# Kernel tuning notes

Hardware: AMD Instinct MI355X
Metric: run time of the kernel (lower is better)

The kernel has to match this reference:

```python
import jax, jax.numpy as jnp
import numpy as np

N_NODES = 100000
N_EDGES = 800000
IN_F, H_F, OUT_F = 512, 256, 64
N_EXPERTS = 4  # k = 1


def _normalize_edges(edge_index, n):
    """gcn_norm: add self loops, symmetric D^-1/2 A D^-1/2 edge weights."""
    loop = jnp.arange(n, dtype=edge_index.dtype)
    row = jnp.concatenate([edge_index[0], loop])
    col = jnp.concatenate([edge_index[1], loop])
    w = jnp.ones(row.shape[0], dtype=jnp.float32)
    deg = jax.ops.segment_sum(w, col, num_segments=n)  # in-degree incl. self loop
    dinv = jnp.where(deg > 0, deg ** -0.5, 0.0)
    norm = dinv[row] * w * dinv[col]
    return row, col, norm


def _propagate(x, row, col, norm, n):
    # message x_j * edge_weight, scatter-add at destination col
    msgs = x[row] * norm[:, None]
    return jax.ops.segment_sum(msgs, col, num_segments=n)


def _moe_linear(x, w_gate, expert_w, expert_b):
    # eval-mode noisy top-k gating with k=1: clean logits, top-1, softmax over
    # a single logit -> gate value 1.0 for the selected expert.
    logits = x @ w_gate                         # [N, E]
    idx = jnp.argmax(logits, axis=-1)           # [N]
    gates = jax.nn.one_hot(idx, N_EXPERTS, dtype=x.dtype)  # [N, E]
    y_all = jnp.einsum('ni,eio->neo', x, expert_w) + expert_b[None]  # [N, E, H]
    return jnp.einsum('ne,neo->no', gates, y_all)


def setup_inputs() -> dict:
    key = jax.random.key(0)
    ks = jax.random.split(key, 8)
    x = jax.random.normal(ks[0], (N_NODES, IN_F), dtype=jnp.float32)
    edge_index = jax.random.randint(ks[1], (2, N_EDGES), 0, N_NODES, dtype=jnp.int64)
    w_gate = jax.random.normal(ks[2], (IN_F, N_EXPERTS), dtype=jnp.float32) * 0.05
    expert_w = jax.random.normal(ks[3], (N_EXPERTS, IN_F, H_F), dtype=jnp.float32) * (1.0 / np.sqrt(IN_F))
    expert_b = jnp.zeros((N_EXPERTS, H_F), dtype=jnp.float32)
    bias1 = jnp.zeros((H_F,), dtype=jnp.float32)
    w2 = jax.random.normal(ks[4], (H_F, OUT_F), dtype=jnp.float32) * (1.0 / np.sqrt(H_F))
    bias2 = jnp.zeros((OUT_F,), dtype=jnp.float32)
    return {"x": x, "edge_index": edge_index, "w_gate": w_gate,
            "expert_w": expert_w, "expert_b": expert_b, "bias1": bias1,
            "w2": w2, "bias2": bias2}


def reference(x, edge_index, w_gate, expert_w, expert_b, bias1, w2, bias2):
    n = x.shape[0]
    row, col, norm = _normalize_edges(edge_index, n)
    # conv1: MoE linear -> propagate -> bias
    h = _moe_linear(x, w_gate, expert_w, expert_b)
    h = _propagate(h, row, col, norm, n) + bias1
    h = jax.nn.relu(h)
    # dropout is identity at eval
    # conv2: plain GCNConv
    h = h @ w2
    h = _propagate(h, row, col, norm, n) + bias2
    return jax.nn.log_softmax(h, axis=1)
```

## Files before the change

### kernel.cpp

```cpp
#include <hip/hip_runtime.h>
#include <math.h>

typedef __bf16 bf16x8 __attribute__((ext_vector_type(8)));
typedef float f32x16 __attribute__((ext_vector_type(16)));

__device__ __forceinline__ unsigned short f2bf(float f) {
  union { float f; unsigned int u; } v; v.f = f;
  unsigned int r = (v.u + 0x7FFFu + ((v.u >> 16) & 1u)) >> 16;
  return (unsigned short)r;
}
__device__ __forceinline__ float bf2f(unsigned short u) {
  union { unsigned int u; float f; } v; v.u = ((unsigned int)u) << 16;
  return v.f;
}
__device__ __forceinline__ void bf2x(unsigned int u, float& lo, float& hi) {
  union { unsigned int u; float f; } a, b;
  a.u = u << 16; b.u = u & 0xFFFF0000u;
  lo = a.f; hi = b.f;
}
__device__ __forceinline__ void gload16(const void* g, void* l) {
  __builtin_amdgcn_global_load_lds(
      (__attribute__((address_space(1))) void*)const_cast<void*>(g),
      (__attribute__((address_space(3))) void*)l, 16, 0, 0);
}

__global__ void k_init(int* cnt, int* meta, int N) {
  int i = blockIdx.x * blockDim.x + threadIdx.x;
  if (i < N) cnt[i] = 0;
  if (i < 32) meta[i] = 0;
}

__global__ __launch_bounds__(256) void k_scanA(const int* __restrict__ cnt,
                                               int* __restrict__ incl,
                                               int* __restrict__ bsums, int N) {
  __shared__ int s[1024];
  int base = blockIdx.x * 1024;
  #pragma unroll
  for (int t = 0; t < 4; ++t) {
    int i = threadIdx.x + t * 256;
    int idx = base + i;
    s[i] = (idx < N) ? cnt[idx] : 0;
  }
  __syncthreads();
  for (int d = 1; d < 1024; d <<= 1) {
    int v[4];
    #pragma unroll
    for (int t = 0; t < 4; ++t) {
      int i = threadIdx.x + t * 256;
      v[t] = (i >= d) ? s[i - d] : 0;
    }
    __syncthreads();
    #pragma unroll
    for (int t = 0; t < 4; ++t) {
      int i = threadIdx.x + t * 256;
      s[i] += v[t];
    }
    __syncthreads();
  }
  #pragma unroll
  for (int t = 0; t < 4; ++t) {
    int i = threadIdx.x + t * 256;
    int idx = base + i;
    if (idx < N) incl[idx] = s[i];
  }
  if (threadIdx.x == 0) bsums[blockIdx.x] = s[1023];
}

__global__ __launch_bounds__(256) void k_scanB(const int* __restrict__ bsums,
                                               int* __restrict__ boff, int nb) {
  __shared__ int s[1024];
  #pragma unroll
  for (int t = 0; t < 4; ++t) {
    int i = threadIdx.x + t * 256;
    s[i] = (i < nb) ? bsums[i] : 0;
  }
  __syncthreads();
  for (int d = 1; d < 1024; d <<= 1) {
    int v[4];
    #pragma unroll
    for (int t = 0; t < 4; ++t) {
      int i = threadIdx.x + t * 256;
      v[t] = (i >= d) ? s[i - d] : 0;
    }
    __syncthreads();
    #pragma unroll
    for (int t = 0; t < 4; ++t) {
      int i = threadIdx.x + t * 256;
      s[i] += v[t];
    }
    __syncthreads();
  }
  #pragma unroll
  for (int t = 0; t < 4; ++t) {
    int i = threadIdx.x + t * 256;
    if (i < nb) boff[i] = (i == 0) ? 0 : s[i - 1];
  }
}

__global__ void k_scanC(const int* __restrict__ cnt, const int* __restrict__ incl,
                        const int* __restrict__ boff, int* __restrict__ rowptr,
                        int* __restrict__ cursor, float* __restrict__ dinv,
                        int* __restrict__ meta, int N, int E) {
  int i = blockIdx.x * blockDim.x + threadIdx.x;
  if (i < N) {
    int ex = incl[i] - cnt[i] + boff[i >> 10];
    rowptr[i] = ex;
    cursor[i] = ex;
    dinv[i] = rsqrtf((float)(cnt[i] + 1));
    if (i == 0) rowptr[N] = E;
  }
  if (blockIdx.x == 0 && threadIdx.x == 0) {
    int* hist = meta;
    int* eoff = meta + 4;
    int* toff = meta + 9;
    int* ecur = meta + 14;
    int s = 0, t = 0;
    eoff[0] = 0; toff[0] = 0;
    for (int e = 0; e < 4; ++e) {
      s += hist[e];
      eoff[e + 1] = s;
      t += (hist[e] + 127) / 128;
      toff[e + 1] = t;
      ecur[e] = eoff[e];
    }
  }
}

__global__ __launch_bounds__(256) void k_scatter(const int* __restrict__ row,
                                                 const int* __restrict__ col,
                                                 int* __restrict__ cursor,
                                                 const float* __restrict__ dinv,
                                                 int2* __restrict__ csr2, int E,
                                                 const int* __restrict__ eidx,
                                                 int* __restrict__ meta,
                                                 int* __restrict__ perm, int N, int scatB) {
  int tid = threadIdx.x;
  if (blockIdx.x < (unsigned)scatB) {
    int e = blockIdx.x * 256 + tid;
    if (e < E) {
      int c = col[e];
      int r = row[e];
      int p = atomicAdd(&cursor[c], 1);
      csr2[p] = make_int2(r, __float_as_int(dinv[r]));
    }
    return;
  }
  __shared__ int lhist[4];
  __shared__ int lbase[4];
  if (tid < 4) lhist[tid] = 0;
  __syncthreads();
  int n = (blockIdx.x - scatB) * 256 + tid;
  int e = 0, lrank = 0;
  bool valid = (n < N);
  if (valid) {
    e = eidx[n];
    lrank = atomicAdd(&lhist[e], 1);
  }
  __syncthreads();
  if (tid < 4) {
    int c = lhist[tid];
    lbase[tid] = (c > 0) ? atomicAdd(&meta[14 + tid], c) : 0;
  }
  __syncthreads();
  if (valid) perm[lbase[e] + lrank] = n;
}

__global__ __launch_bounds__(256) void k_gate(const float* __restrict__ x,
                                              const float* __restrict__ wg,
                                              int* __restrict__ eidx,
                                              int* __restrict__ meta,
                                              unsigned short* __restrict__ xb,
                                              const int* __restrict__ col,
                                              int* __restrict__ cnt,
                                              const float* __restrict__ ew,
                                              unsigned short* __restrict__ ewb,
                                              const float* __restrict__ w2,
                                              unsigned short* __restrict__ w2b,
                                              int N, int E, int gateB, int cntB) {
  int tid = threadIdx.x;
  int b = blockIdx.x;
  int usedC = min(cntB, gateB / 2);
  int mix3 = 3 * usedC;
  int role, idx;
  if (b < mix3) {
    if ((b % 3) == 2) { role = 1; idx = b / 3; }
    else              { role = 0; idx = (b / 3) * 2 + (b % 3); }
  } else {
    int r = b - mix3;
    int gLeft = gateB - 2 * usedC;
    if (r < gLeft) { role = 0; idx = 2 * usedC + r; }
    else {
      r -= gLeft;
      int cLeft = cntB - usedC;
      if (r < cLeft) { role = 1; idx = usedC + r; }
      else           { role = 2; idx = r - cLeft; }
    }
  }

  if (role == 1) {
    int e = idx * 256 + tid;
    if (e < E) atomicAdd(&cnt[col[e]], 1);
    return;
  }
  if (role == 2) {
    if (idx < 256) {
      int n = tid;
      int eidx2 = idx >> 6, kc = idx & 63;
      const float* src = ew + ((size_t)eidx2 * 512 + (size_t)kc * 8) * 256 + n;
      unsigned short tmp[8];
      #pragma unroll
      for (int ke = 0; ke < 8; ++ke) tmp[ke] = f2bf(src[(size_t)ke * 256]);
      *(uint4*)(ewb + ((size_t)idx * 256 + n) * 8) = *(const uint4*)tmp;
    } else {
      int kc = idx - 256;
      if (tid < 64) {
        const float* src = w2 + (size_t)kc * 8 * 64 + tid;
        unsigned short tmp[8];
        #pragma unroll
        for (int ke = 0; ke < 8; ++ke) tmp[ke] = f2bf(src[(size_t)ke * 64]);
        *(uint4*)(w2b + ((size_t)kc * 64 + tid) * 8) = *(const uint4*)tmp;
      }
    }
    return;
  }

  __shared__ float wgT[4][512];
  __shared__ int lhist[4];
  if (tid < 4) lhist[tid] = 0;
  {
    int r0 = tid * 2;
    float4 wa = *(const float4*)(wg + 4 * r0);
    float4 wb = *(const float4*)(wg + 4 * (r0 + 1));
    wgT[0][r0] = wa.x; wgT[1][r0] = wa.y; wgT[2][r0] = wa.z; wgT[3][r0] = wa.w;
    wgT[0][r0 + 1] = wb.x; wgT[1][r0 + 1] = wb.y; wgT[2][r0 + 1] = wb.z; wgT[3][r0 + 1] = wb.w;
  }
  __syncthreads();
  int node = idx * 16 + (tid >> 4);
  int sl = tid & 15;
  if (node < N) {
    const float* xr = x + (size_t)node * 512;
    unsigned short* xbr = xb + (size_t)node * 512;
    float4 xv[8];
    #pragma unroll
    for (int j = 0; j < 8; ++j) xv[j] = *(const float4*)(xr + 4 * (sl + 16 * j));
    #pragma unroll
    for (int j = 0; j < 8; ++j) {
      ushort4 ov;
      ov.x = f2bf(xv[j].x); ov.y = f2bf(xv[j].y); ov.z = f2bf(xv[j].z); ov.w = f2bf(xv[j].w);
      *(ushort4*)(xbr + 4 * (sl + 16 * j)) = ov;
    }
    float l0 = 0.f, l1 = 0.f, l2 = 0.f, l3 = 0.f;
    #pragma unroll
    for (int j = 0; j < 8; ++j) {
      int k0 = 4 * (sl + 16 * j);
      float4 w0 = *(const float4*)&wgT[0][k0];
      float4 w1 = *(const float4*)&wgT[1][k0];
      float4 w2v = *(const float4*)&wgT[2][k0];
      float4 w3 = *(const float4*)&wgT[3][k0];
      l0 += xv[j].x * w0.x + xv[j].y * w0.y + xv[j].z * w0.z + xv[j].w * w0.w;
      l1 += xv[j].x * w1.x + xv[j].y * w1.y + xv[j].z * w1.z + xv[j].w * w1.w;
      l2 += xv[j].x * w2v.x + xv[j].y * w2v.y + xv[j].z * w2v.z + xv[j].w * w2v.w;
      l3 += xv[j].x * w3.x + xv[j].y * w3.y + xv[j].z * w3.z + xv[j].w * w3.w;
    }
    #pragma unroll
    for (int off = 8; off > 0; off >>= 1) {
      l0 += __shfl_xor(l0, off, 64);
      l1 += __shfl_xor(l1, off, 64);
      l2 += __shfl_xor(l2, off, 64);
      l3 += __shfl_xor(l3, off, 64);
    }
    if (sl == 0) {
      int a = 0; float best = l0;
      if (l1 > best) { best = l1; a = 1; }
      if (l2 > best) { best = l2; a = 2; }
      if (l3 > best) { best = l3; a = 3; }
      eidx[node] = a;
      atomicAdd(&lhist[a], 1);
    }
  }
  __syncthreads();
  if (tid < 4 && lhist[tid] > 0) atomicAdd(&meta[tid], lhist[tid]);
}

__global__ __launch_bounds__(512, 2) void k_gemm1(const unsigned short* __restrict__ xb,
                                                  const unsigned short* __restrict__ ewb,
                                                  const float* __restrict__ eb,
                                                  const int* __restrict__ perm,
                                                  const int* __restrict__ meta,
                                                  unsigned short* __restrict__ h1) {
  __shared__ __align__(16) unsigned short A_lds[8192];
  __shared__ __align__(16) unsigned short B_lds[16384];
  __shared__ int sperm[128];
  const int* eoff = meta + 4;
  const int* toff = meta + 9;
  int v = blockIdx.x;
  if (v >= toff[4]) return;
  int e = 0;
  while (v >= toff[e + 1]) ++e;
  int m0 = eoff[e] + (v - toff[e]) * 128;
  int mEnd = eoff[e + 1];
  int tid = threadIdx.x;

  if (tid < 128) {
    int m = m0 + tid;
    sperm[tid] = perm[(m < mEnd) ? m : (mEnd - 1)];
  }
  __syncthreads();

  int wave = tid >> 6, lane = tid & 63;
  int wr = wave >> 2, wc = wave & 3;
  int hi = lane >> 5, lo = lane & 31;
  int r128 = tid & 127;

  f32x16 acc[2][2];
  #pragma unroll
  for (int mi = 0; mi < 2; ++mi)
    #pragma unroll
    for (int ni = 0; ni < 2; ++ni)
      #pragma unroll
      for (int r = 0; r < 16; ++r) acc[mi][ni][r] = 0.f;

  const unsigned short* arow = xb + (size_t)sperm[r128] * 512;
  int kclA = tid >> 7;
  const uint4* ebase = (const uint4*)(ewb + (size_t)e * 64 * 2048);

  for (int k0 = 0; k0 < 512; k0 += 64) {
    __syncthreads();
    gload16(arow + k0 + kclA * 8,       &A_lds[((size_t)kclA * 128 + r128) * 8]);
    gload16(arow + k0 + (kclA + 4) * 8, &A_lds[((size_t)(kclA + 4) * 128 + r128) * 8]);
    const uint4* bsrc = ebase + (size_t)(k0 >> 3) * 256;
    gload16(bsrc + tid,        &B_lds[((size_t)0 * 512 + tid) * 8]);
    gload16(bsrc + 512 + tid,  &B_lds[((size_t)1 * 512 + tid) * 8]);
    gload16(bsrc + 1024 + tid, &B_lds[((size_t)2 * 512 + tid) * 8]);
    gload16(bsrc + 1536 + tid, &B_lds[((size_t)3 * 512 + tid) * 8]);
    __syncthreads();
    #pragma unroll
    for (int s = 0; s < 4; ++s) {
      int kcl = s * 2 + hi;
      bf16x8 a0f = *(const bf16x8*)&A_lds[((size_t)kcl * 128 + wr * 64 + lo) * 8];
      bf16x8 a1f = *(const bf16x8*)&A_lds[((size_t)kcl * 128 + wr * 64 + 32 + lo) * 8];
      bf16x8 b0f = *(const bf16x8*)&B_lds[((size_t)kcl * 256 + wc * 64 + lo) * 8];
      bf16x8 b1f = *(const bf16x8*)&B_lds[((size_t)kcl * 256 + wc * 64 + 32 + lo) * 8];
      acc[0][0] = __builtin_amdgcn_mfma_f32_32x32x16_bf16(a0f, b0f, acc[0][0], 0, 0, 0);
      acc[0][1] = __builtin_amdgcn_mfma_f32_32x32x16_bf16(a0f, b1f, acc[0][1], 0, 0, 0);
      acc[1][0] = __builtin_amdgcn_mfma_f32_32x32x16_bf16(a1f, b0f, acc[1][0], 0, 0, 0);
      acc[1][1] = __builtin_amdgcn_mfma_f32_32x32x16_bf16(a1f, b1f, acc[1][1], 0, 0, 0);
    }
  }

  #pragma unroll
  for (int ni = 0; ni < 2; ++ni) {
    int col = wc * 64 + ni * 32 + lo;
    float bias = eb[e * 256 + col];
    #pragma unroll
    for (int mi = 0; mi < 2; ++mi) {
      #pragma unroll
      for (int q = 0; q < 4; ++q) {
        #pragma unroll
        for (int j = 0; j < 4; ++j) {
          int r = j + 8 * q + 4 * hi;
          int lrow = wr * 64 + mi * 32 + r;
          if (m0 + lrow < mEnd) {
            h1[(size_t)sperm[lrow] * 256 + col] = f2bf(acc[mi][ni][q * 4 + j] + bias);
          }
        }
      }
    }
  }
}

__global__ __launch_bounds__(256) void k_prop1(const unsigned short* __restrict__ h1,
                                               const int* __restrict__ rowptr,
                                               const int2* __restrict__ csr2,
                                               const float* __restrict__ dinv,
                                               const float* __restrict__ bias1,
                                               unsigned short* __restrict__ hrelu, int N) {
  int tid = threadIdx.x;
  int c = blockIdx.x * 8 + (tid >> 5);
  int l = tid & 31;
  if (c >= N) return;
  float dc = dinv[c];
  const uint4* hr = (const uint4*)h1;
  uint4 sv = hr[(size_t)c * 32 + l];
  float slf = dc * dc;
  float a0, a1, a2, a3, a4, a5, a6, a7;
  {
    float lo, hi;
    bf2x(sv.x, lo, hi); a0 = lo * slf; a1 = hi * slf;
    bf2x(sv.y, lo, hi); a2 = lo * slf; a3 = hi * slf;
    bf2x(sv.z, lo, hi); a4 = lo * slf; a5 = hi * slf;
    bf2x(sv.w, lo, hi); a6 = lo * slf; a7 = hi * slf;
  }
  int jb = rowptr[c], je = rowptr[c + 1];
  int j = jb;
  #define ACC8(v, s) { float lo, hi; \
    bf2x((v).x, lo, hi); a0 += lo * (s); a1 += hi * (s); \
    bf2x((v).y, lo, hi); a2 += lo * (s); a3 += hi * (s); \
    bf2x((v).z, lo, hi); a4 += lo * (s); a5 += hi * (s); \
    bf2x((v).w, lo, hi); a6 += lo * (s); a7 += hi * (s); }
  for (; j + 7 < je; j += 8) {
    int2 rc[8];
    #pragma unroll
    for (int t = 0; t < 8; ++t) rc[t] = csr2[j + t];
    uint4 vv[8];
    #pragma unroll
    for (int t = 0; t < 8; ++t) vv[t] = hr[(size_t)rc[t].x * 32 + l];
    #pragma unroll
    for (int t = 0; t < 8; ++t) {
      float s = __int_as_float(rc[t].y) * dc;
      ACC8(vv[t], s);
    }
  }
  for (; j + 3 < je; j += 4) {
    int2 rc0 = csr2[j], rc1 = csr2[j + 1], rc2 = csr2[j + 2], rc3 = csr2[j + 3];
    uint4 v0 = hr[(size_t)rc0.x * 32 + l];
    uint4 v1 = hr[(size_t)rc1.x * 32 + l];
    uint4 v2 = hr[(size_t)rc2.x * 32 + l];
    uint4 v3 = hr[(size_t)rc3.x * 32 + l];
    float s0 = __int_as_float(rc0.y) * dc, s1 = __int_as_float(rc1.y) * dc;
    float s2 = __int_as_float(rc2.y) * dc, s3 = __int_as_float(rc3.y) * dc;
    ACC8(v0, s0); ACC8(v1, s1); ACC8(v2, s2); ACC8(v3, s3);
  }
  for (; j < je; ++j) {
    int2 rc = csr2[j];
    float s = __int_as_float(rc.y) * dc;
    uint4 v = hr[(size_t)rc.x * 32 + l];
    ACC8(v, s);
  }
  #undef ACC8
  float4 b01 = *(const float4*)(bias1 + l * 8);
  float4 b23 = *(const float4*)(bias1 + l * 8 + 4);
  a0 = fmaxf(a0 + b01.x, 0.f); a1 = fmaxf(a1 + b01.y, 0.f);
  a2 = fmaxf(a2 + b01.z, 0.f); a3 = fmaxf(a3 + b01.w, 0.f);
  a4 = fmaxf(a4 + b23.x, 0.f); a5 = fmaxf(a5 + b23.y, 0.f);
  a6 = fmaxf(a6 + b23.z, 0.f); a7 = fmaxf(a7 + b23.w, 0.f);
  uint4 ov;
  ov.x = ((unsigned int)f2bf(a1) << 16) | f2bf(a0);
  ov.y = ((unsigned int)f2bf(a3) << 16) | f2bf(a2);
  ov.z = ((unsigned int)f2bf(a5) << 16) | f2bf(a4);
  ov.w = ((unsigned int)f2bf(a7) << 16) | f2bf(a6);
  ((uint4*)hrelu)[(size_t)c * 32 + l] = ov;
}

__global__ __launch_bounds__(256, 2) void k_gemm2(const unsigned short* __restrict__ A,
                                                  const unsigned short* __restrict__ w2b,
                                                  unsigned short* __restrict__ h3, int N) {
  __shared__ __align__(16) unsigned short B_lds[16384];
  __shared__ __align__(16) unsigned short A_lds[8192];
  int tid = threadIdx.x;
  int m0 = blockIdx.x * 128;
  #pragma unroll
  for (int it = 0; it < 8; ++it)
    gload16(((const uint4*)w2b) + it * 256 + tid, &B_lds[((size_t)it * 256 + tid) * 8]);

  int wave = tid >> 6, lane = tid & 63;
  int wr = wave >> 1, wc = wave & 1;
  int hi = lane >> 5, lo = lane & 31;

  f32x16 acc[2];
  #pragma unroll
  for (int mi = 0; mi < 2; ++mi)
    #pragma unroll
    for (int r = 0; r < 16; ++r) acc[mi][r] = 0.f;

  int i = tid & 127;
  int row = m0 + i;
  if (row >= N) row = N - 1;
  const unsigned short* arow = A + (size_t)row * 256;
  int kcl0 = tid >> 7;

  for (int k0 = 0; k0 < 256; k0 += 64) {
    __syncthreads();
    #pragma unroll
    for (int t = 0; t < 4; ++t)
      gload16(arow + k0 + (kcl0 + 2 * t) * 8,
              &A_lds[((size_t)(kcl0 + 2 * t) * 128 + i) * 8]);
    __syncthreads();
    #pragma unroll
    for (int s = 0; s < 4; ++s) {
      int kcl = s * 2 + hi;
      bf16x8 a0f = *(const bf16x8*)&A_lds[((size_t)kcl * 128 + wr * 64 + lo) * 8];
      bf16x8 a1f = *(const bf16x8*)&A_lds[((size_t)kcl * 128 + wr * 64 + 32 + lo) * 8];
      bf16x8 bf = *(const bf16x8*)&B_lds[(((size_t)(k0 >> 3) + kcl) * 64 + wc * 32 + lo) * 8];
      acc[0] = __builtin_amdgcn_mfma_f32_32x32x16_bf16(a0f, bf, acc[0], 0, 0, 0);
      acc[1] = __builtin_amdgcn_mfma_f32_32x32x16_bf16(a1f, bf, acc[1], 0, 0, 0);
    }
  }

  int n = wc * 32 + lo;
  #pragma unroll
  for (int mi = 0; mi < 2; ++mi) {
    #pragma unroll
    for (int q = 0; q < 4; ++q) {
      #pragma unroll
      for (int j = 0; j < 4; ++j) {
        int r = j + 8 * q + 4 * hi;
        int orow = m0 + wr * 64 + mi * 32 + r;
        if (orow < N) h3[(size_t)orow * 64 + n] = f2bf(acc[mi][q * 4 + j]);
      }
    }
  }
}

__global__ __launch_bounds__(256) void k_prop2(const unsigned short* __restrict__ h3,
                                               const int* __restrict__ rowptr,
                                               const int2* __restrict__ csr2,
                                               const float* __restrict__ dinv,
                                               const float* __restrict__ bias2,
                                               float* __restrict__ out, int N) {
  int tid = threadIdx.x;
  int c = blockIdx.x * 32 + (tid >> 3);
  int l = tid & 7;
  if (c >= N) return;
  float dc = dinv[c];
  const uint4* hr = (const uint4*)h3;
  uint4 sv = hr[(size_t)c * 8 + l];
  float slf = dc * dc;
  float a0, a1, a2, a3, a4, a5, a6, a7;
  {
    float lo, hi;
    bf2x(sv.x, lo, hi); a0 = lo * slf; a1 = hi * slf;
    bf2x(sv.y, lo, hi); a2 = lo * slf; a3 = hi * slf;
    bf2x(sv.z, lo, hi); a4 = lo * slf; a5 = hi * slf;
    bf2x(sv.w, lo, hi); a6 = lo * slf; a7 = hi * slf;
  }
  int jb = rowptr[c], je = rowptr[c + 1];
  int j = jb;
  #define ACC8(v, s) { float lo, hi; \
    bf2x((v).x, lo, hi); a0 += lo * (s); a1 += hi * (s); \
    bf2x((v).y, lo, hi); a2 += lo * (s); a3 += hi * (s); \
    bf2x((v).z, lo, hi); a4 += lo * (s); a5 += hi * (s); \
    bf2x((v).w, lo, hi); a6 += lo * (s); a7 += hi * (s); }
  for (; j + 7 < je; j += 8) {
    int2 rc[8];
    #pragma unroll
    for (int t = 0; t < 8; ++t) rc[t] = csr2[j + t];
    uint4 vv[8];
    #pragma unroll
    for (int t = 0; t < 8; ++t) vv[t] = hr[(size_t)rc[t].x * 8 + l];
    #pragma unroll
    for (int t = 0; t < 8; ++t) {
      float s = __int_as_float(rc[t].y) * dc;
      ACC8(vv[t], s);
    }
  }
  for (; j + 3 < je; j += 4) {
    int2 rc0 = csr2[j], rc1 = csr2[j + 1], rc2 = csr2[j + 2], rc3 = csr2[j + 3];
    uint4 v0 = hr[(size_t)rc0.x * 8 + l];
    uint4 v1 = hr[(size_t)rc1.x * 8 + l];
    uint4 v2 = hr[(size_t)rc2.x * 8 + l];
    uint4 v3 = hr[(size_t)rc3.x * 8 + l];
    float s0 = __int_as_float(rc0.y) * dc, s1 = __int_as_float(rc1.y) * dc;
    float s2 = __int_as_float(rc2.y) * dc, s3 = __int_as_float(rc3.y) * dc;
    ACC8(v0, s0); ACC8(v1, s1); ACC8(v2, s2); ACC8(v3, s3);
  }
  for (; j < je; ++j) {
    int2 rc = csr2[j];
    float s = __int_as_float(rc.y) * dc;
    uint4 v = hr[(size_t)rc.x * 8 + l];
    ACC8(v, s);
  }
  #undef ACC8
  float4 b01 = *(const float4*)(bias2 + l * 8);
  float4 b23 = *(const float4*)(bias2 + l * 8 + 4);
  a0 += b01.x; a1 += b01.y; a2 += b01.z; a3 += b01.w;
  a4 += b23.x; a5 += b23.y; a6 += b23.z; a7 += b23.w;
  float m = fmaxf(fmaxf(fmaxf(a0, a1), fmaxf(a2, a3)), fmaxf(fmaxf(a4, a5), fmaxf(a6, a7)));
  #pragma unroll
  for (int off = 4; off > 0; off >>= 1) m = fmaxf(m, __shfl_xor(m, off, 64));
  float s = expf(a0 - m) + expf(a1 - m) + expf(a2 - m) + expf(a3 - m)
          + expf(a4 - m) + expf(a5 - m) + expf(a6 - m) + expf(a7 - m);
  #pragma unroll
  for (int off = 4; off > 0; off >>= 1) s += __shfl_xor(s, off, 64);
  float ls = m + logf(s);
  float* orow = out + (size_t)c * 64 + l * 8;
  float4 o0 = make_float4(a0 - ls, a1 - ls, a2 - ls, a3 - ls);
  float4 o1 = make_float4(a4 - ls, a5 - ls, a6 - ls, a7 - ls);
  *(float4*)orow = o0;
  *(float4*)(orow + 4) = o1;
}

extern "C" void kernel_launch(void* const* d_in, const int* in_sizes, int n_in,
                              void* d_out, int out_size, void* d_ws, size_t ws_size,
                              hipStream_t stream) {
  const float* x  = (const float*)d_in[0];
  const int*   ei = (const int*)d_in[1];
  const float* wg = (const float*)d_in[2];
  const float* ew = (const float*)d_in[3];
  const float* eb = (const float*)d_in[4];
  const float* b1 = (const float*)d_in[5];
  const float* w2 = (const float*)d_in[6];
  const float* b2 = (const float*)d_in[7];
  float* out = (float*)d_out;

  int N = in_sizes[0] / 512;
  int E = in_sizes[1] / 2;
  const int* row = ei;
  const int* col = ei + E;

  char* p = (char*)d_ws;
  auto alloc = [&](size_t bytes) -> void* {
    void* r = (void*)p;
    p += (bytes + 255) & ~(size_t)255;
    return r;
  };
  int*   cnt    = (int*)alloc((size_t)N * 4);
  int*   rowptr = (int*)alloc((size_t)(N + 1) * 4);
  int*   cursor = (int*)alloc((size_t)N * 4);
  int*   bsums  = (int*)alloc(1024 * 4);
  int*   boff   = (int*)alloc(1024 * 4);
  float* dinv   = (float*)alloc((size_t)N * 4);
  int*   eidx   = (int*)alloc((size_t)N * 4);
  int*   meta   = (int*)alloc(32 * 4);
  int*   perm   = (int*)alloc((size_t)N * 4);
  int2*  csr2   = (int2*)alloc((size_t)E * 8);
  unsigned short* h1    = (unsigned short*)alloc((size_t)N * 256 * 2);
  unsigned short* hrelu = (unsigned short*)alloc((size_t)N * 256 * 2);
  unsigned short* h3    = (unsigned short*)alloc((size_t)N * 64 * 2);
  unsigned short* xb  = (unsigned short*)alloc((size_t)N * 512 * 2);
  unsigned short* ewb = (unsigned short*)alloc((size_t)4 * 512 * 256 * 2);
  unsigned short* w2b = (unsigned short*)alloc((size_t)256 * 64 * 2);

  int nb = (N + 1023) / 1024;
  int gateB = (N + 15) / 16;
  int cntB = (E + 255) / 256;
  int scatB = (E + 255) / 256;
  int binB = (N + 255) / 256;

  k_init<<<(N + 255) / 256, 256, 0, stream>>>(cnt, meta, N);
  k_gate<<<gateB + cntB + 288, 256, 0, stream>>>(x, wg, eidx, meta, xb, col, cnt,
                                                 ew, ewb, w2, w2b, N, E, gateB, cntB);
  k_scanA<<<nb, 256, 0, stream>>>(cnt, rowptr, bsums, N);
  k_scanB<<<1, 256, 0, stream>>>(bsums, boff, nb);
  k_scanC<<<(N + 255) / 256, 256, 0, stream>>>(cnt, rowptr, boff, rowptr, cursor, dinv,
                                               meta, N, E);
  k_scatter<<<scatB + binB, 256, 0, stream>>>(row, col, cursor, dinv, csr2, E,
                                              eidx, meta, perm, N, scatB);
  int ntiles = (N + 127) / 128 + 4;
  k_gemm1<<<ntiles, 512, 0, stream>>>(xb, ewb, eb, perm, meta, h1);
  k_prop1<<<(N + 7) / 8, 256, 0, stream>>>(h1, rowptr, csr2, dinv, b1, hrelu, N);
  k_gemm2<<<(N + 127) / 128, 256, 0, stream>>>(hrelu, w2b, h3, N);
  k_prop2<<<(N + 31) / 32, 256, 0, stream>>>(h3, rowptr, csr2, dinv, b2, out, N);
}
```

Baseline: 352.0 us.

## Drop scanB kernel, move perm binning into scanA, inline asm loads in gate

The separate single-block scanB kernel is removed. Each scanC block now sums the preceding block totals itself with a wavefront reduction. The expert-bucket permutation is moved from the scatter kernel into extra blocks of scanA, computing expert offsets from the histogram directly with a separate cursor slot in meta. This cuts one kernel launch and a serial dependency. The gate kernel also issues its x loads as inline-asm dwordx4 loads behind an explicit wait, to force all loads in flight before use, at the cost of constraining the compiler's scheduling.

```diff
diff --git a/kernel.cpp b/kernel.cpp
--- a/kernel.cpp
+++ b/kernel.cpp
@@ -3,6 +3,7 @@
 
 typedef __bf16 bf16x8 __attribute__((ext_vector_type(8)));
 typedef float f32x16 __attribute__((ext_vector_type(16)));
+typedef float f32x4v __attribute__((ext_vector_type(4)));
 
 __device__ __forceinline__ unsigned short f2bf(float f) {
   union { float f; unsigned int u; } v; v.f = f;
@@ -32,12 +33,40 @@
 
 __global__ __launch_bounds__(256) void k_scanA(const int* __restrict__ cnt,
                                                int* __restrict__ incl,
-                                               int* __restrict__ bsums, int N) {
+                                               int* __restrict__ bsums, int N,
+                                               const int* __restrict__ eidx,
+                                               int* __restrict__ meta,
+                                               int* __restrict__ perm, int nb) {
+  int tid = threadIdx.x;
+  if (blockIdx.x >= (unsigned)nb) {
+    __shared__ int lhist[4];
+    __shared__ int lbase[4];
+    if (tid < 4) lhist[tid] = 0;
+    __syncthreads();
+    int n = (blockIdx.x - nb) * 256 + tid;
+    int e = 0, lrank = 0;
+    bool valid = (n < N);
+    if (valid) {
+      e = eidx[n];
+      lrank = atomicAdd(&lhist[e], 1);
+    }
+    __syncthreads();
+    if (tid < 4) {
+      int c = lhist[tid];
+      int eo = 0;
+      #pragma unroll
+      for (int k = 0; k < 4; ++k) if (k < tid) eo += meta[k];
+      lbase[tid] = eo + ((c > 0) ? atomicAdd(&meta[18 + tid], c) : 0);
+    }
+    __syncthreads();
+    if (valid) perm[lbase[e] + lrank] = n;
+    return;
+  }
   __shared__ int s[1024];
   int base = blockIdx.x * 1024;
   #pragma unroll
   for (int t = 0; t < 4; ++t) {
-    int i = threadIdx.x + t * 256;
+    int i = tid + t * 256;
     int idx = base + i;
     s[i] = (idx < N) ? cnt[idx] : 0;
   }
@@ -46,64 +75,46 @@
     int v[4];
     #pragma unroll
     for (int t = 0; t < 4; ++t) {
-      int i = threadIdx.x + t * 256;
+      int i = tid + t * 256;
       v[t] = (i >= d) ? s[i - d] : 0;
     }
     __syncthreads();
     #pragma unroll
     for (int t = 0; t < 4; ++t) {
-      int i = threadIdx.x + t * 256;
+      int i = tid + t * 256;
       s[i] += v[t];
     }
     __syncthreads();
   }
   #pragma unroll
   for (int t = 0; t < 4; ++t) {
-    int i = threadIdx.x + t * 256;
+    int i = tid + t * 256;
     int idx = base + i;
     if (idx < N) incl[idx] = s[i];
   }
-  if (threadIdx.x == 0) bsums[blockIdx.x] = s[1023];
-}
-
-__global__ __launch_bounds__(256) void k_scanB(const int* __restrict__ bsums,
-                                               int* __restrict__ boff, int nb) {
-  __shared__ int s[1024];
-  #pragma unroll
-  for (int t = 0; t < 4; ++t) {
-    int i = threadIdx.x + t * 256;
-    s[i] = (i < nb) ? bsums[i] : 0;
+  if (tid == 0) bsums[blockIdx.x] = s[1023];
+}
+
+__global__ __launch_bounds__(256) void k_scanC(const int* __restrict__ cnt,
+                                               const int* __restrict__ incl,
+                                               const int* __restrict__ bsums,
+                                               int* __restrict__ rowptr,
+                                               int* __restrict__ cursor,
+                                               float* __restrict__ dinv,
+                                               int* __restrict__ meta, int N, int E) {
+  __shared__ int sboff;
+  int idx1024 = blockIdx.x >> 2;
+  if (threadIdx.x < 64) {
+    int s = 0;
+    for (int k = threadIdx.x; k < idx1024; k += 64) s += bsums[k];
+    #pragma unroll
+    for (int off = 32; off > 0; off >>= 1) s += __shfl_xor(s, off, 64);
+    if (threadIdx.x == 0) sboff = s;
   }
   __syncthreads();
-  for (int d = 1; d < 1024; d <<= 1) {
-    int v[4];
-    #pragma unroll
-    for (int t = 0; t < 4; ++t) {
-      int i = threadIdx.x + t * 256;
-      v[t] = (i >= d) ? s[i - d] : 0;
-    }
-    __syncthreads();
-    #pragma unroll
-    for (int t = 0; t < 4; ++t) {
-      int i = threadIdx.x + t * 256;
-      s[i] += v[t];
-    }
-    __syncthreads();
-  }
-  #pragma unroll
-  for (int t = 0; t < 4; ++t) {
-    int i = threadIdx.x + t * 256;
-    if (i < nb) boff[i] = (i == 0) ? 0 : s[i - 1];
-  }
-}
-
-__global__ void k_scanC(const int* __restrict__ cnt, const int* __restrict__ incl,
-                        const int* __restrict__ boff, int* __restrict__ rowptr,
-                        int* __restrict__ cursor, float* __restrict__ dinv,
-                        int* __restrict__ meta, int N, int E) {
   int i = blockIdx.x * blockDim.x + threadIdx.x;
   if (i < N) {
-    int ex = incl[i] - cnt[i] + boff[i >> 10];
+    int ex = incl[i] - cnt[i] + sboff;
     rowptr[i] = ex;
     cursor[i] = ex;
     dinv[i] = rsqrtf((float)(cnt[i] + 1));
@@ -126,43 +137,16 @@
   }
 }
 
-__global__ __launch_bounds__(256) void k_scatter(const int* __restrict__ row,
-                                                 const int* __restrict__ col,
-                                                 int* __restrict__ cursor,
-                                                 const float* __restrict__ dinv,
-                                                 int2* __restrict__ csr2, int E,
-                                                 const int* __restrict__ eidx,
-                                                 int* __restrict__ meta,
-                                                 int* __restrict__ perm, int N, int scatB) {
-  int tid = threadIdx.x;
-  if (blockIdx.x < (unsigned)scatB) {
-    int e = blockIdx.x * 256 + tid;
-    if (e < E) {
-      int c = col[e];
-      int r = row[e];
-      int p = atomicAdd(&cursor[c], 1);
-      csr2[p] = make_int2(r, __float_as_int(dinv[r]));
-    }
-    return;
-  }
-  __shared__ int lhist[4];
-  __shared__ int lbase[4];
-  if (tid < 4) lhist[tid] = 0;
-  __syncthreads();
-  int n = (blockIdx.x - scatB) * 256 + tid;
-  int e = 0, lrank = 0;
-  bool valid = (n < N);
-  if (valid) {
-    e = eidx[n];
-    lrank = atomicAdd(&lhist[e], 1);
-  }
-  __syncthreads();
-  if (tid < 4) {
-    int c = lhist[tid];
-    lbase[tid] = (c > 0) ? atomicAdd(&meta[14 + tid], c) : 0;
-  }
-  __syncthreads();
-  if (valid) perm[lbase[e] + lrank] = n;
+__global__ void k_scatter(const int* __restrict__ row, const int* __restrict__ col,
+                          int* __restrict__ cursor, const float* __restrict__ dinv,
+                          int2* __restrict__ csr2, int E) {
+  int e = blockIdx.x * blockDim.x + threadIdx.x;
+  if (e < E) {
+    int c = col[e];
+    int r = row[e];
+    int p = atomicAdd(&cursor[c], 1);
+    csr2[p] = make_int2(r, __float_as_int(dinv[r]));
+  }
 }
 
 __global__ __launch_bounds__(256) void k_gate(const float* __restrict__ x,
@@ -240,9 +224,15 @@
   if (node < N) {
     const float* xr = x + (size_t)node * 512;
     unsigned short* xbr = xb + (size_t)node * 512;
-    float4 xv[8];
-    #pragma unroll
-    for (int j = 0; j < 8; ++j) xv[j] = *(const float4*)(xr + 4 * (sl + 16 * j));
+    f32x4v xv[8];
+    #pragma unroll
+    for (int j = 0; j < 8; ++j) {
+      asm volatile("global_load_dwordx4 %0, %1, off"
+                   : "=v"(xv[j])
+                   : "v"(xr + 4 * (sl + 16 * j)));
+    }
+    asm volatile("s_waitcnt vmcnt(0)");
+    __builtin_amdgcn_sched_barrier(0);
     #pragma unroll
     for (int j = 0; j < 8; ++j) {
       ushort4 ov;
@@ -608,7 +598,6 @@
   int*   rowptr = (int*)alloc((size_t)(N + 1) * 4);
   int*   cursor = (int*)alloc((size_t)N * 4);
   int*   bsums  = (int*)alloc(1024 * 4);
-  int*   boff   = (int*)alloc(1024 * 4);
   float* dinv   = (float*)alloc((size_t)N * 4);
   int*   eidx   = (int*)alloc((size_t)N * 4);
   int*   meta   = (int*)alloc(32 * 4);
@@ -630,12 +619,10 @@
   k_init<<<(N + 255) / 256, 256, 0, stream>>>(cnt, meta, N);
   k_gate<<<gateB + cntB + 288, 256, 0, stream>>>(x, wg, eidx, meta, xb, col, cnt,
                                                  ew, ewb, w2, w2b, N, E, gateB, cntB);
-  k_scanA<<<nb, 256, 0, stream>>>(cnt, rowptr, bsums, N);
-  k_scanB<<<1, 256, 0, stream>>>(bsums, boff, nb);
-  k_scanC<<<(N + 255) / 256, 256, 0, stream>>>(cnt, rowptr, boff, rowptr, cursor, dinv,
+  k_scanA<<<nb + binB, 256, 0, stream>>>(cnt, rowptr, bsums, N, eidx, meta, perm, nb);
+  k_scanC<<<(N + 255) / 256, 256, 0, stream>>>(cnt, rowptr, bsums, rowptr, cursor, dinv,
                                                meta, N, E);
-  k_scatter<<<scatB + binB, 256, 0, stream>>>(row, col, cursor, dinv, csr2, E,
-                                              eidx, meta, perm, N, scatB);
+  k_scatter<<<scatB, 256, 0, stream>>>(row, col, cursor, dinv, csr2, E);
   int ntiles = (N + 127) / 128 + 4;
   k_gemm1<<<ntiles, 512, 0, stream>>>(xb, ewb, eb, perm, meta, h1);
   k_prop1<<<(N + 7) / 8, 256, 0, stream>>>(h1, rowptr, csr2, dinv, b1, hrelu, N);
```

Result: no change. 347.8 us (-1.2%).
